# Kernel tuning notes

Hardware: AMD Instinct MI355X
Metric: run time of the kernel (lower is better)

The kernel has to match this reference:

```python
import jax, jax.numpy as jnp
import numpy as np
import math

B, C, H, W, K, HID = 8, 64, 512, 512, 8, 64

def setup_inputs() -> dict:
    key = jax.random.key(0)
    ks = jax.random.split(key, 12)
    s = 0.05  # weight scale
    return {
        "x": jax.random.normal(ks[0], (B, C, H, W), dtype=jnp.float32),
        "w1k": jax.random.normal(ks[1], (1, HID), dtype=jnp.float32) * s,
        "b1k": jax.random.normal(ks[2], (HID,), dtype=jnp.float32) * s,
        "w2k": jax.random.normal(ks[3], (HID, K * K), dtype=jnp.float32) * s,
        "b2k": jax.random.normal(ks[4], (K * K,), dtype=jnp.float32) * s,
        "w1b": jax.random.normal(ks[5], (1, HID), dtype=jnp.float32) * s,
        "b1b": jax.random.normal(ks[6], (HID,), dtype=jnp.float32) * s,
        "w2b": jax.random.normal(ks[7], (HID, 1), dtype=jnp.float32) * s,
        "b2b": jax.random.normal(ks[8], (1,), dtype=jnp.float32) * s,
        "conv_w": jax.random.normal(ks[9], (C, C), dtype=jnp.float32) * s,
        "conv_b": jax.random.normal(ks[10], (C,), dtype=jnp.float32) * s,
    }

def _patch_pos_dist(h, w, k):
    # normalized distance of each KxK patch center from the image center, row-major over (nh, nw)
    nh, nw = h // k, w // k
    cy, cx = h / 2.0, w / 2.0
    max_d = math.sqrt(cy ** 2 + cx ** 2)
    py = jnp.arange(nh, dtype=jnp.float32) * k + k / 2.0
    px = jnp.arange(nw, dtype=jnp.float32) * k + k / 2.0
    d = jnp.sqrt((py - cy)[:, None] ** 2 + (px - cx)[None, :] ** 2) / max_d
    return d.reshape(nh * nw)  # [L]

def reference(x, w1k, b1k, w2k, b2k, w1b, b1b, w2b, b2b, conv_w, conv_b):
    b, c, h, w = x.shape
    kk = w2k.shape[1]
    k = int(round(math.sqrt(kk)))
    nh, nw = h // k, w // k
    L = nh * nw

    d = _patch_pos_dist(h, w, k)[:, None]  # [L, 1]
    # dynamic per-patch-position kernels and bias (exact-erf GELU as in torch default)
    pk = jax.nn.gelu(d @ w1k + b1k, approximate=False) @ w2k + b2k          # [L, K*K]
    pb = (jax.nn.gelu(d @ w1b + b1b, approximate=False) @ w2b + b2b)[:, 0]  # [L]

    # non-overlapping unfold: [B, C, K*K, L], patches row-major over (nh, nw)
    patches = (x.reshape(b, c, nh, k, nw, k)
                 .transpose(0, 1, 2, 4, 3, 5)
                 .reshape(b, c, L, kk)
                 .transpose(0, 1, 3, 2))

    feats = jnp.einsum('bckl,lk->bcl', patches, pk) + pb[None, None, :]     # [B, C, L]
    feats = jnp.einsum('oc,bcl->bol', conv_w, feats) + conv_b[None, :, None]  # 1x1 conv

    mod = patches * feats[:, :, None, :]  # [B, C, K*K, L]

    # fold back (non-overlapping, so a pure reshape/scatter)
    out = (mod.transpose(0, 1, 3, 2)
              .reshape(b, c, nh, nw, k, k)
              .transpose(0, 1, 2, 4, 3, 5)
              .reshape(b, c, h, w))
    return out
```

## Files before the change

### kernel.cpp

```cpp
#include <hip/hip_runtime.h>
#include <math.h>


static __device__ __forceinline__ float gelu_erf(float x) {
    return 0.5f * x * (1.0f + erff(x * 0.70710678118654752f));
}

__global__ __launch_bounds__(256) void afpm_fused(
    const float* __restrict__ x,
    const float* __restrict__ w1k, const float* __restrict__ b1k,
    const float* __restrict__ w2k, const float* __restrict__ b2k,
    const float* __restrict__ w1b, const float* __restrict__ b1b,
    const float* __restrict__ w2b, const float* __restrict__ b2b,
    const float* __restrict__ conv_w, const float* __restrict__ conv_b,
    float* __restrict__ out)
{
    constexpr int C   = 64;
    constexpr int H   = 512;
    constexpr int W   = 512;
    constexpr int HID = 64;
    constexpr int PWG = 4;

    const int tid = threadIdx.x;
    const int pw  = tid & (PWG - 1);
    const int c   = tid >> 2;
    const int pwg = blockIdx.x;
    const int ph  = blockIdx.y;
    const int b   = blockIdx.z;

    const int pw_glob = pwg * PWG + pw;

    __shared__ float gk[PWG][HID];
    __shared__ float gb[PWG][HID];
    __shared__ float pk[PWG][HID];
    __shared__ float f0[C][PWG];
    __shared__ float ft[C][PWG];
    __shared__ float pbs[PWG];

    const size_t base = (((size_t)b * C + c) * H + (size_t)ph * 8) * W
                        + (size_t)pw_glob * 8;
    const float* xp = x + base;
    float4 v[16];
#pragma unroll
    for (int r = 0; r < 8; ++r) {
        v[2 * r + 0] = *(const float4*)(xp + (size_t)r * W);
        v[2 * r + 1] = *(const float4*)(xp + (size_t)r * W + 4);
    }

    const float py = (float)(ph * 8) + 4.0f - 256.0f;
    const float px = (float)(pw_glob * 8) + 4.0f - 256.0f;
    const float dd = sqrtf(py * py + px * px) * (1.0f / 362.03867196751236f);

    {
        const int h = c;
        gk[pw][h] = gelu_erf(dd * w1k[h] + b1k[h]);
        gb[pw][h] = gelu_erf(dd * w1b[h] + b1b[h]);
    }
    __syncthreads();

    {
        const int j = c;
        float s = b2k[j];
#pragma unroll 8
        for (int h = 0; h < HID; ++h)
            s += gk[pw][h] * w2k[h * HID + j];
        pk[pw][j] = s;

        if (c == 0) {
            float t = b2b[0];
            for (int h = 0; h < HID; ++h)
                t += gb[pw][h] * w2b[h];
            pbs[pw] = t;
        }
    }
    __syncthreads();

    {
        float s = 0.0f;
#pragma unroll
        for (int r = 0; r < 8; ++r) {
            const float4 a = v[2 * r + 0];
            const float4 q = v[2 * r + 1];
            s += a.x * pk[pw][r * 8 + 0] + a.y * pk[pw][r * 8 + 1]
               + a.z * pk[pw][r * 8 + 2] + a.w * pk[pw][r * 8 + 3];
            s += q.x * pk[pw][r * 8 + 4] + q.y * pk[pw][r * 8 + 5]
               + q.z * pk[pw][r * 8 + 6] + q.w * pk[pw][r * 8 + 7];
        }
        f0[c][pw] = s + pbs[pw];
    }
    __syncthreads();

    {
        const int o = c;
        float s = conv_b[o];
#pragma unroll 8
        for (int cc = 0; cc < C; ++cc)
            s += conv_w[o * C + cc] * f0[cc][pw];
        ft[o][pw] = s;
    }
    __syncthreads();

    {
        const float m = ft[c][pw];
        float* op = out + base;
#pragma unroll
        for (int r = 0; r < 8; ++r) {
            float4 a = v[2 * r + 0];
            float4 q = v[2 * r + 1];
            a.x *= m; a.y *= m; a.z *= m; a.w *= m;
            q.x *= m; q.y *= m; q.z *= m; q.w *= m;
            *(float4*)(op + (size_t)r * W)     = a;
            *(float4*)(op + (size_t)r * W + 4) = q;
        }
    }
}

extern "C" void kernel_launch(void* const* d_in, const int* in_sizes, int n_in,
                              void* d_out, int out_size, void* d_ws, size_t ws_size,
                              hipStream_t stream) {
    const float* x      = (const float*)d_in[0];
    const float* w1k    = (const float*)d_in[1];
    const float* b1k    = (const float*)d_in[2];
    const float* w2k    = (const float*)d_in[3];
    const float* b2k    = (const float*)d_in[4];
    const float* w1b    = (const float*)d_in[5];
    const float* b1b    = (const float*)d_in[6];
    const float* w2b    = (const float*)d_in[7];
    const float* b2b    = (const float*)d_in[8];
    const float* conv_w = (const float*)d_in[9];
    const float* conv_b = (const float*)d_in[10];
    float* out = (float*)d_out;

    dim3 grid(16, 64, 8);
    afpm_fused<<<grid, 256, 0, stream>>>(x, w1k, b1k, w2k, b2k,
                                         w1b, b1b, w2b, b2b,
                                         conv_w, conv_b, out);
}
```

Baseline: 263.4 us.

## Precompute per-patch MLP kernels once and split patch rows across two threads

Moves the position MLP (GELU plus the 64x64 projection) into a separate small kernel that computes per-patch kernels and biases once per patch position, instead of once per batch element inside every block. The main kernel reads them from the workspace and now uses 512 threads, each loading half a patch row (8 float4s), with a shuffle to combine the partial dot products. This removes redundant MLP work across the batch and lowers register pressure per thread, at the cost of an extra launch and a global round-trip for the kernel table.

```diff
diff --git a/kernel.cpp b/kernel.cpp
--- a/kernel.cpp
+++ b/kernel.cpp
@@ -6,112 +6,120 @@
     return 0.5f * x * (1.0f + erff(x * 0.70710678118654752f));
 }
 
-__global__ __launch_bounds__(256) void afpm_fused(
-    const float* __restrict__ x,
+__global__ __launch_bounds__(256) void mlp_precompute(
     const float* __restrict__ w1k, const float* __restrict__ b1k,
     const float* __restrict__ w2k, const float* __restrict__ b2k,
     const float* __restrict__ w1b, const float* __restrict__ b1b,
     const float* __restrict__ w2b, const float* __restrict__ b2b,
+    float* __restrict__ pk_out,
+    float* __restrict__ pb_out)
+{
+    constexpr int HID = 64;
+    const int tid = threadIdx.x;
+    const int pi  = tid >> 6;
+    const int j   = tid & 63;
+    const int l   = blockIdx.x * 4 + pi;
+
+    const int py_i = l >> 6;
+    const int px_i = l & 63;
+    const float py = (float)(py_i * 8) + 4.0f - 256.0f;
+    const float px = (float)(px_i * 8) + 4.0f - 256.0f;
+    const float dd = sqrtf(py * py + px * px) * (1.0f / 362.03867196751236f);
+
+    __shared__ float gk[4][HID];
+    __shared__ float gb[4][HID];
+
+    gk[pi][j] = gelu_erf(dd * w1k[j] + b1k[j]);
+    gb[pi][j] = gelu_erf(dd * w1b[j] + b1b[j]);
+    __syncthreads();
+
+    float s = b2k[j];
+#pragma unroll 8
+    for (int h = 0; h < HID; ++h)
+        s += gk[pi][h] * w2k[h * HID + j];
+    pk_out[l * HID + j] = s;
+
+    if (j == 0) {
+        float t = b2b[0];
+        for (int h = 0; h < HID; ++h)
+            t += gb[pi][h] * w2b[h];
+        pb_out[l] = t;
+    }
+}
+
+__global__ __launch_bounds__(512) void afpm_main(
+    const float* __restrict__ x,
     const float* __restrict__ conv_w, const float* __restrict__ conv_b,
+    const float* __restrict__ pk_g,
+    const float* __restrict__ pb_g,
     float* __restrict__ out)
 {
     constexpr int C   = 64;
     constexpr int H   = 512;
     constexpr int W   = 512;
-    constexpr int HID = 64;
     constexpr int PWG = 4;
 
     const int tid = threadIdx.x;
-    const int pw  = tid & (PWG - 1);
-    const int c   = tid >> 2;
+    const int q   = tid & 1;
+    const int pw  = (tid >> 1) & 3;
+    const int c   = tid >> 3;
     const int pwg = blockIdx.x;
     const int ph  = blockIdx.y;
     const int b   = blockIdx.z;
 
     const int pw_glob = pwg * PWG + pw;
 
-    __shared__ float gk[PWG][HID];
-    __shared__ float gb[PWG][HID];
-    __shared__ float pk[PWG][HID];
-    __shared__ float f0[C][PWG];
-    __shared__ float ft[C][PWG];
-    __shared__ float pbs[PWG];
+    __shared__ float pkL[PWG][64];
+    __shared__ float pbL[PWG];
+    __shared__ float f0L[C][PWG];
+    __shared__ float ftL[C][PWG];
 
     const size_t base = (((size_t)b * C + c) * H + (size_t)ph * 8) * W
-                        + (size_t)pw_glob * 8;
+                        + (size_t)pw_glob * 8 + (size_t)q * 4;
     const float* xp = x + base;
-    float4 v[16];
+    float4 v[8];
+#pragma unroll
+    for (int r = 0; r < 8; ++r)
+        v[r] = *(const float4*)(xp + (size_t)r * W);
+
+    const int lbase = ph * 64 + pwg * 4;
+    if (tid < 256)
+        pkL[tid >> 6][tid & 63] = pk_g[((size_t)lbase + (tid >> 6)) * 64 + (tid & 63)];
+    else if (tid < 256 + PWG)
+        pbL[tid - 256] = pb_g[lbase + (tid - 256)];
+    __syncthreads();
+
+    float s = 0.0f;
 #pragma unroll
     for (int r = 0; r < 8; ++r) {
-        v[2 * r + 0] = *(const float4*)(xp + (size_t)r * W);
-        v[2 * r + 1] = *(const float4*)(xp + (size_t)r * W + 4);
+        const float4 a = v[r];
+        const int k0 = r * 8 + q * 4;
+        s += a.x * pkL[pw][k0 + 0] + a.y * pkL[pw][k0 + 1]
+           + a.z * pkL[pw][k0 + 2] + a.w * pkL[pw][k0 + 3];
     }
+    s += __shfl_xor(s, 1);
+    if (q == 0)
+        f0L[c][pw] = s + pbL[pw];
+    __syncthreads();
 
-    const float py = (float)(ph * 8) + 4.0f - 256.0f;
-    const float px = (float)(pw_glob * 8) + 4.0f - 256.0f;
-    const float dd = sqrtf(py * py + px * px) * (1.0f / 362.03867196751236f);
-
-    {
-        const int h = c;
-        gk[pw][h] = gelu_erf(dd * w1k[h] + b1k[h]);
-        gb[pw][h] = gelu_erf(dd * w1b[h] + b1b[h]);
+    if (tid < 256) {
+        const int o   = tid >> 2;
+        const int pw2 = tid & 3;
+        float t = conv_b[o];
+#pragma unroll 8
+        for (int cc = 0; cc < C; ++cc)
+            t += conv_w[o * C + cc] * f0L[cc][pw2];
+        ftL[o][pw2] = t;
     }
     __syncthreads();
 
-    {
-        const int j = c;
-        float s = b2k[j];
-#pragma unroll 8
-        for (int h = 0; h < HID; ++h)
-            s += gk[pw][h] * w2k[h * HID + j];
-        pk[pw][j] = s;
-
-        if (c == 0) {
-            float t = b2b[0];
-            for (int h = 0; h < HID; ++h)
-                t += gb[pw][h] * w2b[h];
-            pbs[pw] = t;
-        }
-    }
-    __syncthreads();
-
-    {
-        float s = 0.0f;
+    const float m = ftL[c][pw];
+    float* op = out + base;
 #pragma unroll
-        for (int r = 0; r < 8; ++r) {
-            const float4 a = v[2 * r + 0];
-            const float4 q = v[2 * r + 1];
-            s += a.x * pk[pw][r * 8 + 0] + a.y * pk[pw][r * 8 + 1]
-               + a.z * pk[pw][r * 8 + 2] + a.w * pk[pw][r * 8 + 3];
-            s += q.x * pk[pw][r * 8 + 4] + q.y * pk[pw][r * 8 + 5]
-               + q.z * pk[pw][r * 8 + 6] + q.w * pk[pw][r * 8 + 7];
-        }
-        f0[c][pw] = s + pbs[pw];
-    }
-    __syncthreads();
-
-    {
-        const int o = c;
-        float s = conv_b[o];
-#pragma unroll 8
-        for (int cc = 0; cc < C; ++cc)
-            s += conv_w[o * C + cc] * f0[cc][pw];
-        ft[o][pw] = s;
-    }
-    __syncthreads();
-
-    {
-        const float m = ft[c][pw];
-        float* op = out + base;
-#pragma unroll
-        for (int r = 0; r < 8; ++r) {
-            float4 a = v[2 * r + 0];
-            float4 q = v[2 * r + 1];
-            a.x *= m; a.y *= m; a.z *= m; a.w *= m;
-            q.x *= m; q.y *= m; q.z *= m; q.w *= m;
-            *(float4*)(op + (size_t)r * W)     = a;
-            *(float4*)(op + (size_t)r * W + 4) = q;
-        }
+    for (int r = 0; r < 8; ++r) {
+        float4 a = v[r];
+        a.x *= m; a.y *= m; a.z *= m; a.w *= m;
+        *(float4*)(op + (size_t)r * W) = a;
     }
 }
 
@@ -131,8 +139,13 @@
     const float* conv_b = (const float*)d_in[10];
     float* out = (float*)d_out;
 
+    constexpr int L = 64 * 64;
+    float* pk = (float*)d_ws;
+    float* pb = pk + (size_t)L * 64;
+
+    mlp_precompute<<<L / 4, 256, 0, stream>>>(w1k, b1k, w2k, b2k,
+                                              w1b, b1b, w2b, b2b, pk, pb);
+
     dim3 grid(16, 64, 8);
-    afpm_fused<<<grid, 256, 0, stream>>>(x, w1k, b1k, w2k, b2k,
-                                         w1b, b1b, w2b, b2b,
-                                         conv_w, conv_b, out);
+    afpm_main<<<grid, 512, 0, stream>>>(x, conv_w, conv_b, pk, pb, out);
 }
```

After: 240.8 us. -8.6%, faster.
